# Kernel optimization log

Measured on AMD Instinct MI355X. Metric: run time of the kernel, lower is better.

The kernel has to match this reference:

```python
import jax, jax.numpy as jnp
import numpy as np
import math

B, Q, K, D = 16, 2048, 2048, 128


def setup_inputs() -> dict:
    key = jax.random.key(0)
    kq, kk, kv, kl = jax.random.split(key, 4)
    queries = jax.random.normal(kq, (B, Q, D), dtype=jnp.float32)
    keys = jax.random.normal(kk, (B, K, D), dtype=jnp.float32)
    values = jax.random.normal(kv, (B, K, D), dtype=jnp.float32)
    valid_lens = jax.random.randint(kl, (B,), 1, K + 1, dtype=jnp.int32)
    return {"queries": queries, "keys": keys, "values": values, "valid_lens": valid_lens}


def reference(queries, keys, values, valid_lens):
    d = queries.shape[-1]
    # scores = bmm(Q, K^T) // sqrt(d)  -- source uses floor-division, kept faithfully
    scores = jnp.floor(jnp.einsum('bqd,bkd->bqk', queries, keys) / math.sqrt(d))
    # masked_softmax: positions >= valid_len[b] get -1e6 before softmax
    mask = jnp.arange(keys.shape[1]) < valid_lens[:, None, None]  # [B,1,K]
    scores = jnp.where(mask, scores, -1e6)
    attn = jax.nn.softmax(scores, axis=-1)
    # dropout in eval mode = identity
    return jnp.einsum('bqk,bkv->bqv', attn, values)
```

## Files before the change

kernel.cpp:

```cpp
#include <hip/hip_runtime.h>
#include <cmath>

typedef __attribute__((ext_vector_type(4))) float f32x4;
typedef __attribute__((ext_vector_type(8))) _Float16 f16x8;
typedef __attribute__((ext_vector_type(4))) _Float16 f16x4;

#define B_SZ 16
#define Q_SZ 2048
#define K_SZ 2048
#define D_SZ 128
#define BQ   64
#define BKT  64
#define PST  72
#define SCL  0.08838834764831845f

#define GLDS16(g, s) __builtin_amdgcn_global_load_lds(                      \
    (const __attribute__((address_space(1))) unsigned int*)(g),             \
    (__attribute__((address_space(3))) unsigned int*)(s), 16, 0, 0)

__global__ __launch_bounds__(256) void prep_all(
    const float* __restrict__ K, const float* __restrict__ V,
    _Float16* __restrict__ Khi, _Float16* __restrict__ Klo,
    _Float16* __restrict__ Vt)
{
  __shared__ _Float16 tmp[64][136];
  const int tid = threadIdx.x;
  if (blockIdx.x < 2048) {
    const int gid = blockIdx.x * 256 + tid;
    const int r = gid >> 4;
    const int g = gid & 15;
    const float* src = K + (size_t)r * D_SZ + g * 8;
    f16x8 hi, lo;
#pragma unroll
    for (int i = 0; i < 8; ++i) {
      float x = src[i];
      _Float16 h = (_Float16)x;
      hi[i] = h;
      lo[i] = (_Float16)((x - (float)h) * 2048.0f);
    }
    const size_t o = (size_t)r * D_SZ + ((g ^ (r & 7)) * 8);
    *(f16x8*)(Khi + o) = hi;
    *(f16x8*)(Klo + o) = lo;
  } else {
    const int vb = blockIdx.x - 2048;
    const int b = vb >> 5;
    const int k0 = (vb & 31) * 64;
    const float* Vb = V + ((size_t)b * K_SZ + k0) * D_SZ;
#pragma unroll
    for (int j = 0; j < 8; ++j) {
      const int e = j * 1024 + tid * 4;
      const int k = e >> 7, d = e & 127;
      const f32x4 v = *(const f32x4*)(Vb + (size_t)k * D_SZ + d);
      f16x4 h;
#pragma unroll
      for (int i = 0; i < 4; ++i) h[i] = (_Float16)v[i];
      *(f16x4*)&tmp[k][d] = h;
    }
    __syncthreads();
#pragma unroll
    for (int i = 0; i < 4; ++i) {
      const int id = i * 256 + tid;
      const int gk = id >> 7, d = id & 127;
      f16x8 o;
#pragma unroll
      for (int jj = 0; jj < 8; ++jj) o[jj] = tmp[gk * 8 + jj][d];
      _Float16* dst = Vt + ((size_t)b * D_SZ + d) * K_SZ + k0 + ((gk ^ (d & 7)) * 8);
      *(f16x8*)dst = o;
    }
  }
}

__global__ __launch_bounds__(256, 2) void attn(
    const float* __restrict__ Qm, const _Float16* __restrict__ KhiG,
    const _Float16* __restrict__ KloG, const _Float16* __restrict__ VtG,
    const int* __restrict__ vlp, float* __restrict__ Om,
    float* __restrict__ P1, float* __restrict__ L0, float* __restrict__ L1,
    unsigned* __restrict__ cnt, const int split)
{
  __shared__ __align__(16) char sm[49152 + 64 * PST * 2];
  char* smKhi_c = sm;
  char* smKlo_c = sm + 16384;
  char* smVt_c  = sm + 32768;
  _Float16* smKhi = (_Float16*)smKhi_c;
  _Float16* smKlo = (_Float16*)smKlo_c;
  _Float16* smVt  = (_Float16*)smVt_c;
  _Float16* smP   = (_Float16*)(sm + 49152);
  __shared__ int s_task;
  __shared__ float Ls[2][2][32];

  const int tid  = threadIdx.x;
  const int wave = tid >> 6;
  const int lane = tid & 63;
  const int ln   = lane & 15;
  const int quad = lane >> 4;
  const int qh   = wave >> 1;
  const int kh   = wave & 1;

  for (;;) {
    int t;
    if (split) {
      if (tid == 0) s_task = (int)atomicAdd(cnt, 1u);
      __syncthreads();
      t = s_task;
      __syncthreads();
      if (t >= 1024) return;
    } else {
      t = blockIdx.x;
    }

    int half = 0, b, qt;
    if (split) { half = (t >= 512); const int u = t & 511; b = u >> 5; qt = u & 31; }
    else       { b = t >> 5; qt = t & 31; }
    const int q0     = qt * BQ;
    const int valid  = vlp[b];
    const int kstart = half * 1024;
    const int kend   = split ? min(valid, kstart + 1024) : valid;
    if (kend <= kstart) { if (!split) return; continue; }
    const int ntiles = (kend - kstart + BKT - 1) / BKT;

    const float* Qb    = Qm + (size_t)b * Q_SZ * D_SZ;
    const char*  gKhiB = (const char*)KhiG + (size_t)b * K_SZ * 256;
    const char*  gKloB = (const char*)KloG + (size_t)b * K_SZ * 256;
    const char*  gVtB  = (const char*)VtG  + (size_t)b * D_SZ * (K_SZ * 2);

    f16x8 qhi[2][4], qlo[2][4];
#pragma unroll
    for (int mt = 0; mt < 2; ++mt) {
      const int qrow = q0 + qh * 32 + mt * 16 + ln;
      const float* srcb = Qb + (size_t)qrow * D_SZ + quad * 8;
#pragma unroll
      for (int c = 0; c < 4; ++c) {
#pragma unroll
        for (int j = 0; j < 8; ++j) {
          float x = srcb[c * 32 + j];
          _Float16 h = (_Float16)x;
          qhi[mt][c][j] = h;
          qlo[mt][c][j] = (_Float16)((x - (float)h) * 2048.0f);
        }
      }
    }

    const f32x4 vzero = {0.f, 0.f, 0.f, 0.f};
    f32x4 accO[2][4];
    float lsum[8];
#pragma unroll
    for (int mt = 0; mt < 2; ++mt)
#pragma unroll
      for (int nb = 0; nb < 4; ++nb) accO[mt][nb] = vzero;
#pragma unroll
    for (int i = 0; i < 8; ++i) lsum[i] = 0.0f;

    for (int kt = 0; kt < ntiles; ++kt) {
      const int k0g = kstart + kt * BKT;

      {
        const char* gh = gKhiB + (size_t)k0g * 256;
        const char* gl = gKloB + (size_t)k0g * 256;
#pragma unroll
        for (int i = 0; i < 4; ++i) {
          const int off = (wave * 4 + i) * 1024;
          GLDS16(gh + off + lane * 16, smKhi_c + off);
          GLDS16(gl + off + lane * 16, smKlo_c + off);
        }
#pragma unroll
        for (int i = 0; i < 4; ++i) {
          const int off = (wave * 4 + i) * 1024;
          const int a = off + lane * 16;
          const int d = a >> 7, win = a & 127;
          GLDS16(gVtB + (size_t)d * (K_SZ * 2) + (size_t)k0g * 2 + win, smVt_c + off);
        }
      }
      __syncthreads();

      f32x4 accM[2][2], accC[2][2];
#pragma unroll
      for (int mt = 0; mt < 2; ++mt)
#pragma unroll
        for (int nb = 0; nb < 2; ++nb) { accM[mt][nb] = vzero; accC[mt][nb] = vzero; }
#pragma unroll
      for (int nb = 0; nb < 2; ++nb) {
        const int row = kh * 32 + nb * 16 + ln;
        const _Float16* bh_base = smKhi + row * 128;
        const _Float16* bl_base = smKlo + row * 128;
#pragma unroll
        for (int c = 0; c < 4; ++c) {
          const int pg = (((c * 4 + quad) ^ (ln & 7)) * 8);
          const f16x8 bh = *(const f16x8*)(bh_base + pg);
          const f16x8 bl = *(const f16x8*)(bl_base + pg);
#pragma unroll
          for (int mt = 0; mt < 2; ++mt) {
            accM[mt][nb] = __builtin_amdgcn_mfma_f32_16x16x32_f16(qhi[mt][c], bh, accM[mt][nb], 0, 0, 0);
            accC[mt][nb] = __builtin_amdgcn_mfma_f32_16x16x32_f16(qhi[mt][c], bl, accC[mt][nb], 0, 0, 0);
            accC[mt][nb] = __builtin_amdgcn_mfma_f32_16x16x32_f16(qlo[mt][c], bh, accC[mt][nb], 0, 0, 0);
          }
        }
      }

#pragma unroll
      for (int nb = 0; nb < 2; ++nb) {
        const int  key = k0g + kh * 32 + nb * 16 + ln;
        const bool ok  = key < valid;
#pragma unroll
        for (int mt = 0; mt < 2; ++mt) {
#pragma unroll
          for (int r = 0; r < 4; ++r) {
            const float s = accM[mt][nb][r] + accC[mt][nb][r] * (1.0f / 2048.0f);
            const float e = ok ? __expf(floorf(s * SCL)) : 0.0f;
            lsum[mt * 4 + r] += e;
            smP[(qh * 32 + mt * 16 + quad * 4 + r) * PST + kh * 32 + nb * 16 + ln] = (_Float16)e;
          }
        }
      }
      __syncthreads();

#pragma unroll
      for (int c = 0; c < 2; ++c) {
        f16x8 af[2];
#pragma unroll
        for (int mt = 0; mt < 2; ++mt)
          af[mt] = *(const f16x8*)(smP + (qh * 32 + mt * 16 + ln) * PST + c * 32 + quad * 8);
#pragma unroll
        for (int nb = 0; nb < 4; ++nb) {
          const int drow = kh * 64 + nb * 16 + ln;
          const int pg = (((c * 4 + quad) ^ (ln & 7)) * 8);
          const f16x8 bf = *(const f16x8*)(smVt + drow * 64 + pg);
#pragma unroll
          for (int mt = 0; mt < 2; ++mt)
            accO[mt][nb] = __builtin_amdgcn_mfma_f32_16x16x32_f16(af[mt], bf, accO[mt][nb], 0, 0, 0);
        }
      }
      __syncthreads();
    }

#pragma unroll
    for (int i = 0; i < 8; ++i) {
      float v = lsum[i];
      v += __shfl_xor(v, 1, 64);
      v += __shfl_xor(v, 2, 64);
      v += __shfl_xor(v, 4, 64);
      v += __shfl_xor(v, 8, 64);
      lsum[i] = v;
    }

    if (split) {
      float* Lh = half ? L1 : L0;
      if (ln == 0) {
#pragma unroll
        for (int mt = 0; mt < 2; ++mt)
#pragma unroll
          for (int r = 0; r < 4; ++r)
            atomicAdd(Lh + b * Q_SZ + q0 + qh * 32 + mt * 16 + quad * 4 + r, lsum[mt * 4 + r]);
      }
      float* dst = (half ? P1 : Om) + ((size_t)(b * Q_SZ + q0)) * D_SZ;
#pragma unroll
      for (int mt = 0; mt < 2; ++mt)
#pragma unroll
        for (int nb = 0; nb < 4; ++nb)
#pragma unroll
          for (int r = 0; r < 4; ++r)
            dst[(size_t)(qh * 32 + mt * 16 + quad * 4 + r) * D_SZ + kh * 64 + nb * 16 + ln] =
                accO[mt][nb][r];
    } else {
      if (ln == 0) {
#pragma unroll
        for (int mt = 0; mt < 2; ++mt)
#pragma unroll
          for (int r = 0; r < 4; ++r)
            Ls[qh][kh][mt * 16 + quad * 4 + r] = lsum[mt * 4 + r];
      }
      __syncthreads();
      float* Ob = Om + (size_t)b * Q_SZ * D_SZ;
#pragma unroll
      for (int mt = 0; mt < 2; ++mt) {
#pragma unroll
        for (int r = 0; r < 4; ++r) {
          const int rr = mt * 16 + quad * 4 + r;
          const float inv = 1.0f / (Ls[qh][0][rr] + Ls[qh][1][rr]);
#pragma unroll
          for (int nb = 0; nb < 4; ++nb)
            Ob[(size_t)(q0 + qh * 32 + rr) * D_SZ + kh * 64 + nb * 16 + ln] =
                accO[mt][nb][r] * inv;
        }
      }
    }
    if (!split) return;
  }
}

__global__ __launch_bounds__(256) void finalize(
    float* __restrict__ Om, const float* __restrict__ P1,
    const float* __restrict__ L0, const float* __restrict__ L1,
    const int* __restrict__ vlp)
{
  const int idx = blockIdx.x * 256 + threadIdx.x;
  const size_t e = (size_t)idx * 4;
  const int row = (int)(e >> 7);
  const int b = row >> 11;
  const int valid = vlp[b];
  f32x4 o = *(const f32x4*)(Om + e);
  float l = L0[row];
  if (valid > 1024) {
    const f32x4 p = *(const f32x4*)(P1 + e);
    o += p;
    l += L1[row];
  }
  const float inv = 1.0f / l;
  o *= inv;
  *(f32x4*)(Om + e) = o;
}

extern "C" void kernel_launch(void* const* d_in, const int* in_sizes, int n_in,
                              void* d_out, int out_size, void* d_ws, size_t ws_size,
                              hipStream_t stream) {
  const float* Qm = (const float*)d_in[0];
  const float* Km = (const float*)d_in[1];
  const float* Vm = (const float*)d_in[2];
  const int*   vl = (const int*)d_in[3];
  float*       Om = (float*)d_out;

  const size_t elems = (size_t)B_SZ * K_SZ * D_SZ;
  const size_t PREP  = 3 * elems * sizeof(_Float16);
  const size_t HDR   = 262400;
  const size_t P1SZ  = elems * sizeof(float);
  char* W = (char*)d_ws;

  if (ws_size >= HDR + PREP + P1SZ) {
    unsigned* cnt = (unsigned*)W;
    float*    L0  = (float*)(W + 256);
    float*    L1  = (float*)(W + 256 + 131072);
    _Float16* Khi = (_Float16*)(W + HDR);
    _Float16* Klo = Khi + elems;
    _Float16* Vt  = Klo + elems;
    float*    P1  = (float*)(W + HDR + PREP);
    hipMemsetAsync(d_ws, 0, HDR, stream);
    prep_all<<<2560, 256, 0, stream>>>(Km, Vm, Khi, Klo, Vt);
    attn<<<512, 256, 0, stream>>>(Qm, Khi, Klo, Vt, vl, Om, P1, L0, L1, cnt, 1);
    finalize<<<4096, 256, 0, stream>>>(Om, P1, L0, L1, vl);
  } else {
    _Float16* Khi = (_Float16*)W;
    _Float16* Klo = Khi + elems;
    _Float16* Vt  = Klo + elems;
    prep_all<<<2560, 256, 0, stream>>>(Km, Vm, Khi, Klo, Vt);
    attn<<<512, 256, 0, stream>>>(Qm, Khi, Klo, Vt, vl, Om,
                                  nullptr, nullptr, nullptr, nullptr, 0);
  }
}
```

Before: 168.4 us.

## Double-buffer K/V tiles with async LDS loads and enlarge query tile to 128

The attention kernel now prefetches the next K-hi, K-lo and V^T tile into a second LDS buffer while the current tile is computed. It waits with explicit vmcnt and raw s_barrier calls instead of full __syncthreads. The query tile grows to 128 rows with 512-thread blocks and 8 waves, halving the task count, and MFMA sections run at raised wave priority. The aim is to hide global-to-LDS latency and reuse each staged K/V tile across more queries. In exchange, LDS use rises to about 114 KB per block, which likely allows only one block per CU, and the split scheduling has coarser tasks.

```diff
diff --git a/kernel.cpp b/kernel.cpp
--- a/kernel.cpp
+++ b/kernel.cpp
@@ -9,10 +9,11 @@
 #define Q_SZ 2048
 #define K_SZ 2048
 #define D_SZ 128
-#define BQ   64
+#define BQ   128
 #define BKT  64
 #define PST  72
 #define SCL  0.08838834764831845f
+#define BUFSZ 49152
 
 #define GLDS16(g, s) __builtin_amdgcn_global_load_lds(                      \
     (const __attribute__((address_space(1))) unsigned int*)(g),             \
@@ -70,23 +71,17 @@
   }
 }
 
-__global__ __launch_bounds__(256, 2) void attn(
+__global__ __launch_bounds__(512, 2) void attn(
     const float* __restrict__ Qm, const _Float16* __restrict__ KhiG,
     const _Float16* __restrict__ KloG, const _Float16* __restrict__ VtG,
     const int* __restrict__ vlp, float* __restrict__ Om,
     float* __restrict__ P1, float* __restrict__ L0, float* __restrict__ L1,
     unsigned* __restrict__ cnt, const int split)
 {
-  __shared__ __align__(16) char sm[49152 + 64 * PST * 2];
-  char* smKhi_c = sm;
-  char* smKlo_c = sm + 16384;
-  char* smVt_c  = sm + 32768;
-  _Float16* smKhi = (_Float16*)smKhi_c;
-  _Float16* smKlo = (_Float16*)smKlo_c;
-  _Float16* smVt  = (_Float16*)smVt_c;
-  _Float16* smP   = (_Float16*)(sm + 49152);
+  __shared__ __align__(16) char sm[2 * BUFSZ + BQ * PST * 2];
+  _Float16* smP = (_Float16*)(sm + 2 * BUFSZ);
   __shared__ int s_task;
-  __shared__ float Ls[2][2][32];
+  __shared__ float Ls[4][2][32];
 
   const int tid  = threadIdx.x;
   const int wave = tid >> 6;
@@ -103,14 +98,14 @@
       __syncthreads();
       t = s_task;
       __syncthreads();
-      if (t >= 1024) return;
+      if (t >= 512) return;
     } else {
       t = blockIdx.x;
     }
 
     int half = 0, b, qt;
-    if (split) { half = (t >= 512); const int u = t & 511; b = u >> 5; qt = u & 31; }
-    else       { b = t >> 5; qt = t & 31; }
+    if (split) { half = (t >= 256); const int u = t & 255; b = u >> 4; qt = u & 15; }
+    else       { b = t >> 4; qt = t & 15; }
     const int q0     = qt * BQ;
     const int valid  = vlp[b];
     const int kstart = half * 1024;
@@ -123,6 +118,29 @@
     const char*  gKloB = (const char*)KloG + (size_t)b * K_SZ * 256;
     const char*  gVtB  = (const char*)VtG  + (size_t)b * D_SZ * (K_SZ * 2);
 
+    auto STAGE = [&](int k0g, char* buf) {
+      const char* gh = gKhiB + (size_t)k0g * 256;
+      const char* gl = gKloB + (size_t)k0g * 256;
+#pragma unroll
+      for (int i = 0; i < 2; ++i) {
+        const int off = wave * 1024 + i * 8192;
+        GLDS16(gh + off + lane * 16, buf + off);
+      }
+#pragma unroll
+      for (int i = 0; i < 2; ++i) {
+        const int off = wave * 1024 + i * 8192;
+        GLDS16(gl + off + lane * 16, buf + 16384 + off);
+      }
+#pragma unroll
+      for (int i = 0; i < 2; ++i) {
+        const int off = wave * 1024 + i * 8192;
+        const int a = off + lane * 16;
+        const int d = a >> 7, win = a & 127;
+        GLDS16(gVtB + (size_t)d * (K_SZ * 2) + (size_t)k0g * 2 + win,
+               buf + 32768 + off);
+      }
+    };
+
     f16x8 qhi[2][4], qlo[2][4];
 #pragma unroll
     for (int mt = 0; mt < 2; ++mt) {
@@ -150,33 +168,31 @@
 #pragma unroll
     for (int i = 0; i < 8; ++i) lsum[i] = 0.0f;
 
+    STAGE(kstart, sm);
+
     for (int kt = 0; kt < ntiles; ++kt) {
+      char* cbuf = sm + (kt & 1) * BUFSZ;
+      _Float16* smKhi = (_Float16*)cbuf;
+      _Float16* smKlo = (_Float16*)(cbuf + 16384);
+      _Float16* smVt  = (_Float16*)(cbuf + 32768);
       const int k0g = kstart + kt * BKT;
 
-      {
-        const char* gh = gKhiB + (size_t)k0g * 256;
-        const char* gl = gKloB + (size_t)k0g * 256;
-#pragma unroll
-        for (int i = 0; i < 4; ++i) {
-          const int off = (wave * 4 + i) * 1024;
-          GLDS16(gh + off + lane * 16, smKhi_c + off);
-          GLDS16(gl + off + lane * 16, smKlo_c + off);
-        }
-#pragma unroll
-        for (int i = 0; i < 4; ++i) {
-          const int off = (wave * 4 + i) * 1024;
-          const int a = off + lane * 16;
-          const int d = a >> 7, win = a & 127;
-          GLDS16(gVtB + (size_t)d * (K_SZ * 2) + (size_t)k0g * 2 + win, smVt_c + off);
-        }
-      }
-      __syncthreads();
+      if (kt + 1 < ntiles) {
+        STAGE(kstart + (kt + 1) * BKT, sm + ((kt + 1) & 1) * BUFSZ);
+        asm volatile("s_waitcnt vmcnt(6)" ::: "memory");
+      } else {
+        asm volatile("s_waitcnt vmcnt(0)" ::: "memory");
+      }
+      __builtin_amdgcn_sched_barrier(0);
+      __builtin_amdgcn_s_barrier();
+      __builtin_amdgcn_sched_barrier(0);
 
       f32x4 accM[2][2], accC[2][2];
 #pragma unroll
       for (int mt = 0; mt < 2; ++mt)
 #pragma unroll
         for (int nb = 0; nb < 2; ++nb) { accM[mt][nb] = vzero; accC[mt][nb] = vzero; }
+      __builtin_amdgcn_s_setprio(1);
 #pragma unroll
       for (int nb = 0; nb < 2; ++nb) {
         const int row = kh * 32 + nb * 16 + ln;
@@ -195,6 +211,7 @@
           }
         }
       }
+      __builtin_amdgcn_s_setprio(0);
 
 #pragma unroll
       for (int nb = 0; nb < 2; ++nb) {
@@ -211,8 +228,12 @@
           }
         }
       }
-      __syncthreads();
-
+      asm volatile("s_waitcnt lgkmcnt(0)" ::: "memory");
+      __builtin_amdgcn_sched_barrier(0);
+      __builtin_amdgcn_s_barrier();
+      __builtin_amdgcn_sched_barrier(0);
+
+      __builtin_amdgcn_s_setprio(1);
 #pragma unroll
       for (int c = 0; c < 2; ++c) {
         f16x8 af[2];
@@ -229,7 +250,11 @@
             accO[mt][nb] = __builtin_amdgcn_mfma_f32_16x16x32_f16(af[mt], bf, accO[mt][nb], 0, 0, 0);
         }
       }
-      __syncthreads();
+      __builtin_amdgcn_s_setprio(0);
+      asm volatile("s_waitcnt lgkmcnt(0)" ::: "memory");
+      __builtin_amdgcn_sched_barrier(0);
+      __builtin_amdgcn_s_barrier();
+      __builtin_amdgcn_sched_barrier(0);
     }
 
 #pragma unroll
@@ -334,14 +359,14 @@
     float*    P1  = (float*)(W + HDR + PREP);
     hipMemsetAsync(d_ws, 0, HDR, stream);
     prep_all<<<2560, 256, 0, stream>>>(Km, Vm, Khi, Klo, Vt);
-    attn<<<512, 256, 0, stream>>>(Qm, Khi, Klo, Vt, vl, Om, P1, L0, L1, cnt, 1);
+    attn<<<256, 512, 0, stream>>>(Qm, Khi, Klo, Vt, vl, Om, P1, L0, L1, cnt, 1);
     finalize<<<4096, 256, 0, stream>>>(Om, P1, L0, L1, vl);
   } else {
     _Float16* Khi = (_Float16*)W;
     _Float16* Klo = Khi + elems;
     _Float16* Vt  = Klo + elems;
     prep_all<<<2560, 256, 0, stream>>>(Km, Vm, Khi, Klo, Vt);
-    attn<<<512, 256, 0, stream>>>(Qm, Khi, Klo, Vt, vl, Om,
+    attn<<<256, 512, 0, stream>>>(Qm, Khi, Klo, Vt, vl, Om,
                                   nullptr, nullptr, nullptr, nullptr, 0);
   }
 }
```

New measurement: 172.3 us. 1.02x slower.
